# Optimization experiments

Measured on AMD Instinct MI355X. Metric: run time of the kernel, lower is better.

Reference implementation:

```python
import jax, jax.numpy as jnp
import numpy as np

EPS = 1e-5
K = 3
N_TAP = K * K


def _bn(x, g, b, m, v):
    # eval-mode batchnorm over channel axis 1 of NCHW
    inv = g / jnp.sqrt(v + EPS)
    return x * inv[None, :, None, None] + (b - m * inv)[None, :, None, None]


def _silu(x):
    return x * jax.nn.sigmoid(x)


def _dcn(x, offset, mask, w, b, pad=1):
    """Modulated deformable conv (DCNv2), stride 1.
    x: [B,C,H,W], offset: [B,2n,H,W] ((dy,dx) per tap), mask: [B,n,H,W],
    w: [O,C,K,K], b: [O]."""
    B, C, H, W = x.shape
    O = w.shape[0]
    ky, kx = jnp.meshgrid(jnp.arange(K), jnp.arange(K), indexing='ij')
    ky = ky.reshape(N_TAP).astype(x.dtype)
    kx = kx.reshape(N_TAP).astype(x.dtype)
    off = offset.reshape(B, N_TAP, 2, H, W)
    base_y = jnp.arange(H, dtype=x.dtype)[None, None, :, None]
    base_x = jnp.arange(W, dtype=x.dtype)[None, None, None, :]
    # fractional sample positions [B,n,H,W]
    py = base_y - pad + ky[None, :, None, None] + off[:, :, 0]
    px = base_x - pad + kx[None, :, None, None] + off[:, :, 1]
    y0 = jnp.floor(py)
    x0 = jnp.floor(px)
    fy = py - y0
    fx = px - x0
    y0i = y0.astype(jnp.int32)
    x0i = x0.astype(jnp.int32)
    x_flat = x.reshape(B, C, 1, H * W)

    def corner(yi, xi, wgt):
        valid = (yi >= 0) & (yi < H) & (xi >= 0) & (xi < W)
        idx = (jnp.clip(yi, 0, H - 1) * W + jnp.clip(xi, 0, W - 1)).reshape(B, 1, N_TAP, H * W)
        v = jnp.take_along_axis(x_flat, idx, axis=-1)  # [B,C,n,HW]
        return v * (wgt * valid.astype(x.dtype)).reshape(B, 1, N_TAP, H * W)

    acc = corner(y0i, x0i, (1 - fy) * (1 - fx))
    acc = acc + corner(y0i, x0i + 1, (1 - fy) * fx)
    acc = acc + corner(y0i + 1, x0i, fy * (1 - fx))
    acc = acc + corner(y0i + 1, x0i + 1, fy * fx)
    val = acc.reshape(B, C, N_TAP, H, W) * mask[:, None]  # modulation
    out = jnp.einsum('bcnhw,ocn->bohw', val, w.reshape(O, C, N_TAP))
    return out + b[None, :, None, None]


def setup_inputs() -> dict:
    key = jax.random.key(0)
    ks = jax.random.split(key, 16)
    B, C1, H, W = 8, 256, 80, 80
    C2 = 256
    Ch = 128  # c_ = int(c2 * 0.5)
    d = {}
    d['x'] = jax.random.normal(ks[0], (B, C1, H, W), jnp.float32)
    # cv1: 1x1 conv (no bias) + BN
    d['cv1_w'] = jax.random.normal(ks[1], (Ch, C1), jnp.float32) * (1.0 / np.sqrt(C1))
    d['bn1_g'] = jax.random.uniform(ks[2], (Ch,), jnp.float32, 0.5, 1.5)
    d['bn1_b'] = jax.random.normal(ks[3], (Ch,), jnp.float32) * 0.1
    d['bn1_m'] = jax.random.normal(ks[4], (Ch,), jnp.float32) * 0.1
    d['bn1_v'] = jax.random.uniform(ks[5], (Ch,), jnp.float32, 0.5, 1.5)
    # offset/mask predictor 3x3 conv (small weights -> modest deformation)
    d['off_w'] = jax.random.normal(ks[6], (3 * N_TAP, Ch, K, K), jnp.float32) * 0.01
    d['off_b'] = jnp.zeros((3 * N_TAP,), jnp.float32)
    # dcn main weight/bias
    d['dcn_w'] = jax.random.normal(ks[7], (Ch, Ch, K, K), jnp.float32) * (1.0 / np.sqrt(Ch * N_TAP))
    d['dcn_b'] = jnp.zeros((Ch,), jnp.float32)
    d['bn2_g'] = jax.random.uniform(ks[8], (Ch,), jnp.float32, 0.5, 1.5)
    d['bn2_b'] = jax.random.normal(ks[9], (Ch,), jnp.float32) * 0.1
    d['bn2_m'] = jax.random.normal(ks[10], (Ch,), jnp.float32) * 0.1
    d['bn2_v'] = jax.random.uniform(ks[11], (Ch,), jnp.float32, 0.5, 1.5)
    # cv2: 1x1 conv (no bias) + BN
    d['cv2_w'] = jax.random.normal(ks[12], (C2, Ch), jnp.float32) * (1.0 / np.sqrt(Ch))
    d['bn3_g'] = jax.random.uniform(ks[13], (C2,), jnp.float32, 0.5, 1.5)
    d['bn3_b'] = jax.random.normal(ks[14], (C2,), jnp.float32) * 0.1
    d['bn3_m'] = jax.random.normal(ks[15], (C2,), jnp.float32) * 0.1
    d['bn3_v'] = jnp.ones((C2,), jnp.float32)
    return d


def reference(x, cv1_w, bn1_g, bn1_b, bn1_m, bn1_v,
              off_w, off_b, dcn_w, dcn_b, bn2_g, bn2_b, bn2_m, bn2_v,
              cv2_w, bn3_g, bn3_b, bn3_m, bn3_v):
    # cv1: 1x1 conv -> BN -> SiLU
    y = _silu(_bn(jnp.einsum('bchw,oc->bohw', x, cv1_w), bn1_g, bn1_b, bn1_m, bn1_v))
    # offset/mask predictor: 3x3 conv, pad 1
    raw = jax.lax.conv_general_dilated(
        y, off_w, window_strides=(1, 1), padding=((1, 1), (1, 1)),
        dimension_numbers=('NCHW', 'OIHW', 'NCHW')) + off_b[None, :, None, None]
    offset = raw[:, :2 * N_TAP]
    mask = jax.nn.sigmoid(raw[:, 2 * N_TAP:])
    # modulated deformable 3x3 conv -> BN -> SiLU
    y = _silu(_bn(_dcn(y, offset, mask, dcn_w, dcn_b), bn2_g, bn2_b, bn2_m, bn2_v))
    # cv2: 1x1 conv -> BN -> SiLU
    y = _silu(_bn(jnp.einsum('bchw,oc->bohw', y, cv2_w), bn3_g, bn3_b, bn3_m, bn3_v))
    return x + y  # shortcut (c1 == c2)
```

## Files before the change

kernel.cpp:

```cpp
#include <hip/hip_runtime.h>
#include <math.h>

#define HWSZ 6400
#define WIMG 80
#define HIMG 80
#define BEPS 1e-5f

typedef __attribute__((ext_vector_type(8))) short short8;
typedef __attribute__((ext_vector_type(4))) short s16x4;
typedef __attribute__((ext_vector_type(4))) float f32x4;
typedef __attribute__((ext_vector_type(4))) int i32x4;

__device__ __forceinline__ unsigned short f2b(float f) {
    unsigned u = __builtin_bit_cast(unsigned, f);
    u += 0x7fffu + ((u >> 16) & 1u);
    return (unsigned short)(u >> 16);
}
__device__ __forceinline__ int f2b_pk(float flo, float fhi) {
    unsigned lo = __builtin_bit_cast(unsigned, flo);
    unsigned hi = __builtin_bit_cast(unsigned, fhi);
    lo += 0x7fffu + ((lo >> 16) & 1u);
    hi += 0x7fffu + ((hi >> 16) & 1u);
    return (int)__builtin_amdgcn_perm(hi, lo, 0x07060302u);
}
__device__ __forceinline__ float b2f(unsigned short h) {
    unsigned u = ((unsigned)h) << 16;
    return __builtin_bit_cast(float, u);
}
__device__ __forceinline__ float silu_f(float t) { return t / (1.f + __expf(-t)); }

#define BPOS(sub, nt, n16, q) (((((sub)*4 + (nt))*16 + (n16))*40) + (q)*8)
#define BPOS32(sub, nt, n16, oct) (((((sub)*2 + (nt))*16 + (n16))*40) + (oct)*8)

__global__ __launch_bounds__(256) void k_prep(
    const float* __restrict__ cv1w, const float* __restrict__ g1, const float* __restrict__ b1,
    const float* __restrict__ m1, const float* __restrict__ v1,
    const float* __restrict__ offw, const float* __restrict__ offb,
    const float* __restrict__ dcnw, const float* __restrict__ dcnb,
    const float* __restrict__ g2, const float* __restrict__ b2,
    const float* __restrict__ m2, const float* __restrict__ v2,
    const float* __restrict__ cv2w, const float* __restrict__ g3, const float* __restrict__ b3,
    const float* __restrict__ m3, const float* __restrict__ v3,
    unsigned short* __restrict__ apk1, unsigned short* __restrict__ apko,
    unsigned short* __restrict__ apkd, unsigned short* __restrict__ apk2,
    float* __restrict__ bias1, float* __restrict__ biaso,
    float* __restrict__ bias2, float* __restrict__ bias3)
{
    int idx = blockIdx.x * 256 + threadIdx.x;
    if (idx < 32768) {
        int j = idx & 7, L = (idx >> 3) & 63, ks = (idx >> 9) & 7, mt = idx >> 12;
        int o = mt * 16 + (L & 15), k = ks * 32 + (L >> 4) * 8 + j;
        float inv = g1[o] * rsqrtf(v1[o] + BEPS);
        apk1[idx] = f2b(cv1w[o * 256 + k] * inv);
    } else if (idx < 69632) {
        int t = idx - 32768;
        int j = t & 7, L = (t >> 3) & 63;
        int mt = t / 18432, rem = t % 18432, ks = rem >> 9;
        int o = mt * 16 + (L & 15);
        int kp = ks * 32 + (L >> 4) * 8 + j;
        int n = kp >> 7, c = kp & 127;
        float wv = (o < 27) ? offw[(size_t)(o * 128 + c) * 9 + n] : 0.f;
        apko[t] = f2b(wv);
    } else if (idx < 217088) {
        int t = idx - 69632;
        int j = t & 7, L = (t >> 3) & 63;
        int mt = t / 18432, rem = t % 18432, ks = rem >> 9;
        int o = mt * 16 + (L & 15);
        int kp = ks * 32 + (L >> 4) * 8 + j;
        int n = kp >> 7, c = kp & 127;
        float inv = g2[o] * rsqrtf(v2[o] + BEPS);
        apkd[t] = f2b(dcnw[(size_t)(o * 128 + c) * 9 + n] * inv);
    } else if (idx < 249856) {
        int t = idx - 217088;
        int j = t & 7, L = (t >> 3) & 63, ks = (t >> 9) & 3, mt = t >> 11;
        int o = mt * 16 + (L & 15), k = ks * 32 + (L >> 4) * 8 + j;
        float inv = g3[o] * rsqrtf(v3[o] + BEPS);
        apk2[t] = f2b(cv2w[o * 128 + k] * inv);
    } else if (idx < 250395) {
        int t = idx - 249856;
        if (t < 128) { float inv = g1[t] * rsqrtf(v1[t] + BEPS); bias1[t] = b1[t] - m1[t] * inv; }
        else if (t < 155) { biaso[t - 128] = offb[t - 128]; }
        else if (t < 283) { int o = t - 155; float inv = g2[o] * rsqrtf(v2[o] + BEPS);
                            bias2[o] = dcnb[o] * inv + b2[o] - m2[o] * inv; }
        else { int o = t - 283; float inv = g3[o] * rsqrtf(v3[o] + BEPS); bias3[o] = b3[o] - m3[o] * inv; }
    }
}

__global__ __launch_bounds__(256) void k_cv1(
    const float* __restrict__ x, const unsigned short* __restrict__ apk1,
    const float* __restrict__ bias1, unsigned short* __restrict__ y1t)
{
    int blk = blockIdx.x;
    int b = blk & 7, pt = blk >> 3;
    int p0 = pt * 64;
    int tid = threadIdx.x;
    int lane = tid & 63, w = tid >> 6;
    int n16 = lane & 15, qd = lane >> 4;
    int px = p0 + w * 16 + n16;
    const float* xb = x + (size_t)b * 256 * HWSZ + px;
    f32x4 acc[8];
#pragma unroll
    for (int mt = 0; mt < 8; ++mt) acc[mt] = (f32x4){0.f, 0.f, 0.f, 0.f};
#pragma unroll
    for (int ks = 0; ks < 8; ++ks) {
        float xv[8];
#pragma unroll
        for (int j = 0; j < 8; ++j)
            xv[j] = xb[(size_t)(ks * 32 + qd * 8 + j) * HWSZ];
        i32x4 bi;
#pragma unroll
        for (int t = 0; t < 4; ++t) bi[t] = f2b_pk(xv[2 * t], xv[2 * t + 1]);
        short8 bf = __builtin_bit_cast(short8, bi);
#pragma unroll
        for (int mt = 0; mt < 8; ++mt) {
            short8 af = *(const short8*)&apk1[(size_t)((mt * 8 + ks) * 64 + lane) * 8];
            acc[mt] = __builtin_amdgcn_mfma_f32_16x16x32_bf16(af, bf, acc[mt], 0, 0, 0);
        }
    }
    unsigned short* ytb = y1t + ((size_t)b * HWSZ + px) * 128;
#pragma unroll
    for (int mt = 0; mt < 8; ++mt) {
        int o0 = mt * 16 + qd * 4;
        s16x4 v;
#pragma unroll
        for (int r = 0; r < 4; ++r)
            v[r] = (short)f2b(silu_f(acc[mt][r] + bias1[o0 + r]));
        *(s16x4*)&ytb[o0] = v;
    }
}

__global__ __launch_bounds__(256) void k_off(
    const unsigned short* __restrict__ y1t, const unsigned short* __restrict__ apko,
    const float* __restrict__ biaso, float* __restrict__ raw)
{
    int blk = blockIdx.x;
    int b = blk & 7, pt = blk >> 3;
    int p0 = pt * 64;
    int tid = threadIdx.x;
    int lane = tid & 63, w = tid >> 6;
    int n16 = lane & 15, qd = lane >> 4;
    int pxl = w * 16 + n16;
    int p = p0 + pxl;
    int h = p / WIMG, wx = p % WIMG;
    const unsigned short* yb = y1t + (size_t)b * HWSZ * 128 + qd * 8;
    f32x4 acc[2];
    acc[0] = (f32x4){0.f, 0.f, 0.f, 0.f};
    acc[1] = (f32x4){0.f, 0.f, 0.f, 0.f};
    const short8 zz = {0, 0, 0, 0, 0, 0, 0, 0};
#pragma unroll
    for (int n = 0; n < 9; ++n) {
        int hh = h - 1 + n / 3, ww = wx - 1 + n % 3;
        bool valid = ((unsigned)hh < HIMG) && ((unsigned)ww < WIMG);
        int spx = valid ? hh * WIMG + ww : 0;
        const unsigned short* ys = yb + (size_t)spx * 128;
        short8 v[4];
#pragma unroll
        for (int sub = 0; sub < 4; ++sub) {
            v[sub] = *(const short8*)&ys[sub * 32];
            if (!valid) v[sub] = zz;
        }
#pragma unroll
        for (int sub = 0; sub < 4; ++sub) {
            int ks = n * 4 + sub;
            short8 af0 = *(const short8*)&apko[(size_t)(ks * 64 + lane) * 8];
            short8 af1 = *(const short8*)&apko[(size_t)((36 + ks) * 64 + lane) * 8];
            acc[0] = __builtin_amdgcn_mfma_f32_16x16x32_bf16(af0, v[sub], acc[0], 0, 0, 0);
            acc[1] = __builtin_amdgcn_mfma_f32_16x16x32_bf16(af1, v[sub], acc[1], 0, 0, 0);
        }
    }
    float* rb = raw + (size_t)b * 27 * HWSZ + p0 + w * 16 + n16;
#pragma unroll
    for (int mi = 0; mi < 2; ++mi)
#pragma unroll
        for (int r = 0; r < 4; ++r) {
            int o = mi * 16 + qd * 4 + r;
            if (o < 27) {
                float t = acc[mi][r] + biaso[o];
                if (o >= 18) t = 1.f / (1.f + __expf(-t));
                rb[(size_t)o * HWSZ] = t;
            }
        }
}

__global__ __launch_bounds__(256) void k_dcn(
    const unsigned short* __restrict__ y1t, const float* __restrict__ raw,
    const unsigned short* __restrict__ apkd, const float* __restrict__ bias2,
    unsigned short* __restrict__ zt)
{
    __shared__ float swgt[4][9][32];
    __shared__ unsigned short sidx[4][9][32];
    __shared__ __align__(16) unsigned short sV[5120];
    int blk = blockIdx.x;
    int b = blk & 7, pt = blk >> 3;
    int p0 = pt * 32;
    int tid = threadIdx.x;

    for (int i = tid; i < 288; i += 256) {
        int n = i >> 5, pp = i & 31;
        int p = p0 + pp;
        int h = p / WIMG, wx = p % WIMG;
        const float* rb = raw + (size_t)b * 27 * HWSZ + p;
        float dy = rb[(size_t)(2 * n) * HWSZ];
        float dx = rb[(size_t)(2 * n + 1) * HWSZ];
        float mk = rb[(size_t)(18 + n) * HWSZ];
        float py = (float)(h - 1 + n / 3) + dy;
        float px = (float)(wx - 1 + n % 3) + dx;
        float y0f = floorf(py), x0f = floorf(px);
        float fy = py - y0f, fx = px - x0f;
        int y0 = (int)y0f, x0 = (int)x0f;
#pragma unroll
        for (int k = 0; k < 4; ++k) {
            int yy = y0 + (k >> 1);
            int xx = x0 + (k & 1);
            bool valid = ((unsigned)yy < HIMG) && ((unsigned)xx < WIMG);
            float wk = ((k >> 1) ? fy : 1.f - fy) * ((k & 1) ? fx : 1.f - fx);
            wk = valid ? wk * mk : 0.f;
            int yc = min(max(yy, 0), HIMG - 1);
            int xc = min(max(xx, 0), WIMG - 1);
            sidx[k][n][pp] = (unsigned short)(yc * WIMG + xc);
            swgt[k][n][pp] = wk;
        }
    }
    __syncthreads();

    int lane = tid & 63, w = tid >> 6;
    int n16 = lane & 15, qd = lane >> 4;
    int pxl = tid >> 3, q8 = tid & 7;
    int gsub = q8 >> 1;
    int goct = (q8 & 1) * 2;
    const unsigned short* yb = y1t + (size_t)b * HWSZ * 128;
    f32x4 acc[2][2];
#pragma unroll
    for (int mi = 0; mi < 2; ++mi)
#pragma unroll
        for (int nt = 0; nt < 2; ++nt) acc[mi][nt] = (f32x4){0.f, 0.f, 0.f, 0.f};

    for (int n = 0; n < 9; ++n) {
        float av[2][8];
#pragma unroll
        for (int s = 0; s < 2; ++s)
#pragma unroll
            for (int j = 0; j < 8; ++j) av[s][j] = 0.f;
#pragma unroll
        for (int k = 0; k < 4; ++k) {
            float wk = swgt[k][n][pxl];
            const unsigned short* ys = yb + (size_t)sidx[k][n][pxl] * 128 + q8 * 16;
            short8 v0 = *(const short8*)&ys[0];
            short8 v1 = *(const short8*)&ys[8];
#pragma unroll
            for (int j = 0; j < 8; ++j) {
                av[0][j] = fmaf(wk, b2f((unsigned short)v0[j]), av[0][j]);
                av[1][j] = fmaf(wk, b2f((unsigned short)v1[j]), av[1][j]);
            }
        }
#pragma unroll
        for (int s = 0; s < 2; ++s) {
            short8 v;
#pragma unroll
            for (int j = 0; j < 8; ++j) v[j] = (short)f2b(av[s][j]);
            *(short8*)&sV[BPOS32(gsub, pxl >> 4, pxl & 15, goct + s)] = v;
        }
        __syncthreads();
#pragma unroll
        for (int sub = 0; sub < 4; ++sub) {
            int ks = n * 4 + sub;
            short8 bf[2];
#pragma unroll
            for (int nt = 0; nt < 2; ++nt)
                bf[nt] = *(const short8*)&sV[BPOS32(sub, nt, n16, qd)];
#pragma unroll
            for (int mi = 0; mi < 2; ++mi) {
                short8 af = *(const short8*)&apkd[(size_t)(((2 * w + mi) * 36 + ks) * 64 + lane) * 8];
#pragma unroll
                for (int nt = 0; nt < 2; ++nt)
                    acc[mi][nt] = __builtin_amdgcn_mfma_f32_16x16x32_bf16(af, bf[nt], acc[mi][nt], 0, 0, 0);
            }
        }
        __syncthreads();
    }
    unsigned short* zb = zt + ((size_t)b * HWSZ + p0) * 128;
#pragma unroll
    for (int mi = 0; mi < 2; ++mi)
#pragma unroll
        for (int nt = 0; nt < 2; ++nt) {
            int o0 = (2 * w + mi) * 16 + qd * 4;
            int px = nt * 16 + n16;
            s16x4 v;
#pragma unroll
            for (int r = 0; r < 4; ++r)
                v[r] = (short)f2b(silu_f(acc[mi][nt][r] + bias2[o0 + r]));
            *(s16x4*)&zb[(size_t)px * 128 + o0] = v;
        }
}

__global__ __launch_bounds__(256) void k_cv2(
    const unsigned short* __restrict__ zt, const float* __restrict__ x,
    const unsigned short* __restrict__ apk2, const float* __restrict__ bias3,
    float* __restrict__ out)
{
    int blk = blockIdx.x;
    int b = blk & 7, pt = blk >> 3;
    int p0 = pt * 32;
    int tid = threadIdx.x;
    int lane = tid & 63, w = tid >> 6;
    int n16 = lane & 15, qd = lane >> 4;
    const unsigned short* zb = zt + ((size_t)b * HWSZ + p0) * 128;
    f32x4 acc[2][4];
#pragma unroll
    for (int mt = 0; mt < 2; ++mt)
#pragma unroll
        for (int ntl = 0; ntl < 4; ++ntl) acc[mt][ntl] = (f32x4){0.f, 0.f, 0.f, 0.f};
#pragma unroll
    for (int ks = 0; ks < 4; ++ks) {
        short8 az[2];
#pragma unroll
        for (int mt = 0; mt < 2; ++mt)
            az[mt] = *(const short8*)&zb[(size_t)(mt * 16 + n16) * 128 + ks * 32 + qd * 8];
#pragma unroll
        for (int ntl = 0; ntl < 4; ++ntl) {
            int nt = w * 4 + ntl;
            short8 bw = *(const short8*)&apk2[(size_t)((nt * 4 + ks) * 64 + lane) * 8];
#pragma unroll
            for (int mt = 0; mt < 2; ++mt)
                acc[mt][ntl] = __builtin_amdgcn_mfma_f32_16x16x32_bf16(az[mt], bw, acc[mt][ntl], 0, 0, 0);
        }
    }
    const float* xb = x + (size_t)b * 256 * HWSZ;
    float* ob = out + (size_t)b * 256 * HWSZ;
#pragma unroll
    for (int mt = 0; mt < 2; ++mt) {
        int px = p0 + mt * 16 + qd * 4;
#pragma unroll
        for (int ntl = 0; ntl < 4; ++ntl) {
            int o = (w * 4 + ntl) * 16 + n16;
            float bv = bias3[o];
            size_t base = (size_t)o * HWSZ + px;
            float4 xv = *(const float4*)&xb[base];
            float4 r;
            r.x = xv.x + silu_f(acc[mt][ntl][0] + bv);
            r.y = xv.y + silu_f(acc[mt][ntl][1] + bv);
            r.z = xv.z + silu_f(acc[mt][ntl][2] + bv);
            r.w = xv.w + silu_f(acc[mt][ntl][3] + bv);
            *(float4*)&ob[base] = r;
        }
    }
}

extern "C" void kernel_launch(void* const* d_in, const int* in_sizes, int n_in,
                              void* d_out, int out_size, void* d_ws, size_t ws_size,
                              hipStream_t stream) {
    const float* x     = (const float*)d_in[0];
    const float* cv1w  = (const float*)d_in[1];
    const float* bn1g  = (const float*)d_in[2];
    const float* bn1b  = (const float*)d_in[3];
    const float* bn1m  = (const float*)d_in[4];
    const float* bn1v  = (const float*)d_in[5];
    const float* offw  = (const float*)d_in[6];
    const float* offb  = (const float*)d_in[7];
    const float* dcnw  = (const float*)d_in[8];
    const float* dcnb  = (const float*)d_in[9];
    const float* bn2g  = (const float*)d_in[10];
    const float* bn2b  = (const float*)d_in[11];
    const float* bn2m  = (const float*)d_in[12];
    const float* bn2v  = (const float*)d_in[13];
    const float* cv2w  = (const float*)d_in[14];
    const float* bn3g  = (const float*)d_in[15];
    const float* bn3b  = (const float*)d_in[16];
    const float* bn3m  = (const float*)d_in[17];
    const float* bn3v  = (const float*)d_in[18];
    float* out = (float*)d_out;

    float* base = (float*)d_ws;
    unsigned short* y1t = (unsigned short*)base;
    float* raw   = base + 3276800;
    unsigned short* zt  = (unsigned short*)(base + 4659200);
    unsigned short* apk1 = (unsigned short*)(base + 7936000);
    unsigned short* apko = (unsigned short*)(base + 7952384);
    unsigned short* apkd = (unsigned short*)(base + 7970816);
    unsigned short* apk2 = (unsigned short*)(base + 8044544);
    float* bias1 = base + 8060928;
    float* biaso = base + 8061056;
    float* bias2 = base + 8061088;
    float* bias3 = base + 8061216;

    k_prep<<<979, 256, 0, stream>>>(cv1w, bn1g, bn1b, bn1m, bn1v,
                                    offw, offb, dcnw, dcnb,
                                    bn2g, bn2b, bn2m, bn2v,
                                    cv2w, bn3g, bn3b, bn3m, bn3v,
                                    apk1, apko, apkd, apk2,
                                    bias1, biaso, bias2, bias3);
    k_cv1<<<800, 256, 0, stream>>>(x, apk1, bias1, y1t);
    k_off<<<800, 256, 0, stream>>>(y1t, apko, biaso, raw);
    k_dcn<<<1600, 256, 0, stream>>>(y1t, raw, apkd, bias2, zt);
    k_cv2<<<1600, 256, 0, stream>>>(zt, x, apk2, bias3, out);
}
```

Baseline: 239.1 us.

## Fuse offset conv into DCN kernel and triple-buffer gathered taps

Moves the offset/mask 3x3 conv into the DCN kernel: two waves compute the 27 raw channels for the block's 32 pixels into shared memory. This removes the separate kernel launch and the global round-trip of the raw buffer. The tap loop is also restructured with a 3-slot shared buffer so the gather for the next tap overlaps the MFMAs of the current one, and one barrier per tap is dropped. The LDS layout gets a per-sub pad to avoid bank conflicts. The cost is that two of the four waves do the offset conv while the other two sit idle, and LDS use per block grows.

```diff
diff --git a/kernel.cpp b/kernel.cpp
--- a/kernel.cpp
+++ b/kernel.cpp
@@ -29,8 +29,8 @@
 }
 __device__ __forceinline__ float silu_f(float t) { return t / (1.f + __expf(-t)); }
 
-#define BPOS(sub, nt, n16, q) (((((sub)*4 + (nt))*16 + (n16))*40) + (q)*8)
-#define BPOS32(sub, nt, n16, oct) (((((sub)*2 + (nt))*16 + (n16))*40) + (oct)*8)
+#define BPOS32(sub, nt, n16, oct) (((((sub)*2 + (nt))*16 + (n16))*40) + (oct)*8 + (sub)*8)
+#define SVBUF 5184
 
 __global__ __launch_bounds__(256) void k_prep(
     const float* __restrict__ cv1w, const float* __restrict__ g1, const float* __restrict__ b1,
@@ -129,80 +129,75 @@
     }
 }
 
-__global__ __launch_bounds__(256) void k_off(
-    const unsigned short* __restrict__ y1t, const unsigned short* __restrict__ apko,
-    const float* __restrict__ biaso, float* __restrict__ raw)
-{
-    int blk = blockIdx.x;
-    int b = blk & 7, pt = blk >> 3;
-    int p0 = pt * 64;
-    int tid = threadIdx.x;
-    int lane = tid & 63, w = tid >> 6;
-    int n16 = lane & 15, qd = lane >> 4;
-    int pxl = w * 16 + n16;
-    int p = p0 + pxl;
-    int h = p / WIMG, wx = p % WIMG;
-    const unsigned short* yb = y1t + (size_t)b * HWSZ * 128 + qd * 8;
-    f32x4 acc[2];
-    acc[0] = (f32x4){0.f, 0.f, 0.f, 0.f};
-    acc[1] = (f32x4){0.f, 0.f, 0.f, 0.f};
-    const short8 zz = {0, 0, 0, 0, 0, 0, 0, 0};
-#pragma unroll
-    for (int n = 0; n < 9; ++n) {
-        int hh = h - 1 + n / 3, ww = wx - 1 + n % 3;
-        bool valid = ((unsigned)hh < HIMG) && ((unsigned)ww < WIMG);
-        int spx = valid ? hh * WIMG + ww : 0;
-        const unsigned short* ys = yb + (size_t)spx * 128;
-        short8 v[4];
-#pragma unroll
-        for (int sub = 0; sub < 4; ++sub) {
-            v[sub] = *(const short8*)&ys[sub * 32];
-            if (!valid) v[sub] = zz;
-        }
-#pragma unroll
-        for (int sub = 0; sub < 4; ++sub) {
-            int ks = n * 4 + sub;
-            short8 af0 = *(const short8*)&apko[(size_t)(ks * 64 + lane) * 8];
-            short8 af1 = *(const short8*)&apko[(size_t)((36 + ks) * 64 + lane) * 8];
-            acc[0] = __builtin_amdgcn_mfma_f32_16x16x32_bf16(af0, v[sub], acc[0], 0, 0, 0);
-            acc[1] = __builtin_amdgcn_mfma_f32_16x16x32_bf16(af1, v[sub], acc[1], 0, 0, 0);
-        }
-    }
-    float* rb = raw + (size_t)b * 27 * HWSZ + p0 + w * 16 + n16;
-#pragma unroll
-    for (int mi = 0; mi < 2; ++mi)
-#pragma unroll
-        for (int r = 0; r < 4; ++r) {
-            int o = mi * 16 + qd * 4 + r;
-            if (o < 27) {
-                float t = acc[mi][r] + biaso[o];
-                if (o >= 18) t = 1.f / (1.f + __expf(-t));
-                rb[(size_t)o * HWSZ] = t;
-            }
-        }
-}
-
 __global__ __launch_bounds__(256) void k_dcn(
-    const unsigned short* __restrict__ y1t, const float* __restrict__ raw,
+    const unsigned short* __restrict__ y1t,
+    const unsigned short* __restrict__ apko, const float* __restrict__ biaso,
     const unsigned short* __restrict__ apkd, const float* __restrict__ bias2,
     unsigned short* __restrict__ zt)
 {
+    __shared__ float rawL[27 * 33];
     __shared__ float swgt[4][9][32];
     __shared__ unsigned short sidx[4][9][32];
-    __shared__ __align__(16) unsigned short sV[5120];
+    __shared__ __align__(16) unsigned short sV[3 * SVBUF];
     int blk = blockIdx.x;
     int b = blk & 7, pt = blk >> 3;
     int p0 = pt * 32;
     int tid = threadIdx.x;
+    int lane = tid & 63, w = tid >> 6;
+    int n16 = lane & 15, qd = lane >> 4;
+    const unsigned short* yb = y1t + (size_t)b * HWSZ * 128;
+
+    if (w < 2) {
+        int pxa = w * 16 + n16;
+        int p = p0 + pxa;
+        int h = p / WIMG, wx = p % WIMG;
+        const unsigned short* ybq = yb + qd * 8;
+        f32x4 oacc[2];
+        oacc[0] = (f32x4){0.f, 0.f, 0.f, 0.f};
+        oacc[1] = (f32x4){0.f, 0.f, 0.f, 0.f};
+        const short8 zz = {0, 0, 0, 0, 0, 0, 0, 0};
+#pragma unroll
+        for (int n = 0; n < 9; ++n) {
+            int hh = h - 1 + n / 3, ww = wx - 1 + n % 3;
+            bool valid = ((unsigned)hh < HIMG) && ((unsigned)ww < WIMG);
+            int spx = valid ? hh * WIMG + ww : 0;
+            const unsigned short* ys = ybq + (size_t)spx * 128;
+            short8 v[4];
+#pragma unroll
+            for (int sub = 0; sub < 4; ++sub) {
+                v[sub] = *(const short8*)&ys[sub * 32];
+                if (!valid) v[sub] = zz;
+            }
+#pragma unroll
+            for (int sub = 0; sub < 4; ++sub) {
+                int ks = n * 4 + sub;
+                short8 af0 = *(const short8*)&apko[(size_t)(ks * 64 + lane) * 8];
+                short8 af1 = *(const short8*)&apko[(size_t)((36 + ks) * 64 + lane) * 8];
+                oacc[0] = __builtin_amdgcn_mfma_f32_16x16x32_bf16(af0, v[sub], oacc[0], 0, 0, 0);
+                oacc[1] = __builtin_amdgcn_mfma_f32_16x16x32_bf16(af1, v[sub], oacc[1], 0, 0, 0);
+            }
+        }
+#pragma unroll
+        for (int mi = 0; mi < 2; ++mi)
+#pragma unroll
+            for (int r = 0; r < 4; ++r) {
+                int o = mi * 16 + qd * 4 + r;
+                if (o < 27) {
+                    float t = oacc[mi][r] + biaso[o];
+                    if (o >= 18) t = 1.f / (1.f + __expf(-t));
+                    rawL[o * 33 + pxa] = t;
+                }
+            }
+    }
+    __syncthreads();
 
     for (int i = tid; i < 288; i += 256) {
         int n = i >> 5, pp = i & 31;
         int p = p0 + pp;
         int h = p / WIMG, wx = p % WIMG;
-        const float* rb = raw + (size_t)b * 27 * HWSZ + p;
-        float dy = rb[(size_t)(2 * n) * HWSZ];
-        float dx = rb[(size_t)(2 * n + 1) * HWSZ];
-        float mk = rb[(size_t)(18 + n) * HWSZ];
+        float dy = rawL[(2 * n) * 33 + pp];
+        float dx = rawL[(2 * n + 1) * 33 + pp];
+        float mk = rawL[(18 + n) * 33 + pp];
         float py = (float)(h - 1 + n / 3) + dy;
         float px = (float)(wx - 1 + n % 3) + dx;
         float y0f = floorf(py), x0f = floorf(px);
@@ -223,24 +218,19 @@
     }
     __syncthreads();
 
-    int lane = tid & 63, w = tid >> 6;
-    int n16 = lane & 15, qd = lane >> 4;
     int pxl = tid >> 3, q8 = tid & 7;
     int gsub = q8 >> 1;
     int goct = (q8 & 1) * 2;
-    const unsigned short* yb = y1t + (size_t)b * HWSZ * 128;
     f32x4 acc[2][2];
 #pragma unroll
     for (int mi = 0; mi < 2; ++mi)
 #pragma unroll
         for (int nt = 0; nt < 2; ++nt) acc[mi][nt] = (f32x4){0.f, 0.f, 0.f, 0.f};
 
-    for (int n = 0; n < 9; ++n) {
-        float av[2][8];
-#pragma unroll
-        for (int s = 0; s < 2; ++s)
-#pragma unroll
-            for (int j = 0; j < 8; ++j) av[s][j] = 0.f;
+    auto gather_tap = [&](int n, int bsel) {
+        float av0[8], av1[8];
+#pragma unroll
+        for (int j = 0; j < 8; ++j) { av0[j] = 0.f; av1[j] = 0.f; }
 #pragma unroll
         for (int k = 0; k < 4; ++k) {
             float wk = swgt[k][n][pxl];
@@ -249,25 +239,30 @@
             short8 v1 = *(const short8*)&ys[8];
 #pragma unroll
             for (int j = 0; j < 8; ++j) {
-                av[0][j] = fmaf(wk, b2f((unsigned short)v0[j]), av[0][j]);
-                av[1][j] = fmaf(wk, b2f((unsigned short)v1[j]), av[1][j]);
-            }
-        }
-#pragma unroll
-        for (int s = 0; s < 2; ++s) {
-            short8 v;
-#pragma unroll
-            for (int j = 0; j < 8; ++j) v[j] = (short)f2b(av[s][j]);
-            *(short8*)&sV[BPOS32(gsub, pxl >> 4, pxl & 15, goct + s)] = v;
-        }
+                av0[j] = fmaf(wk, b2f((unsigned short)v0[j]), av0[j]);
+                av1[j] = fmaf(wk, b2f((unsigned short)v1[j]), av1[j]);
+            }
+        }
+        short8 o0, o1;
+#pragma unroll
+        for (int j = 0; j < 8; ++j) { o0[j] = (short)f2b(av0[j]); o1[j] = (short)f2b(av1[j]); }
+        unsigned short* dst = &sV[bsel * SVBUF + BPOS32(gsub, pxl >> 4, pxl & 15, goct)];
+        *(short8*)dst = o0;
+        *(short8*)(dst + 8) = o1;
+    };
+
+    gather_tap(0, 0);
+    for (int n = 0; n < 9; ++n) {
+        if (n < 8) gather_tap(n + 1, (n + 1) % 3);
         __syncthreads();
+        int bb = (n % 3) * SVBUF;
 #pragma unroll
         for (int sub = 0; sub < 4; ++sub) {
             int ks = n * 4 + sub;
             short8 bf[2];
 #pragma unroll
             for (int nt = 0; nt < 2; ++nt)
-                bf[nt] = *(const short8*)&sV[BPOS32(sub, nt, n16, qd)];
+                bf[nt] = *(const short8*)&sV[bb + BPOS32(sub, nt, n16, qd)];
 #pragma unroll
             for (int mi = 0; mi < 2; ++mi) {
                 short8 af = *(const short8*)&apkd[(size_t)(((2 * w + mi) * 36 + ks) * 64 + lane) * 8];
@@ -276,8 +271,8 @@
                     acc[mi][nt] = __builtin_amdgcn_mfma_f32_16x16x32_bf16(af, bf[nt], acc[mi][nt], 0, 0, 0);
             }
         }
-        __syncthreads();
-    }
+    }
+
     unsigned short* zb = zt + ((size_t)b * HWSZ + p0) * 128;
 #pragma unroll
     for (int mi = 0; mi < 2; ++mi)
@@ -372,16 +367,15 @@
 
     float* base = (float*)d_ws;
     unsigned short* y1t = (unsigned short*)base;
-    float* raw   = base + 3276800;
-    unsigned short* zt  = (unsigned short*)(base + 4659200);
-    unsigned short* apk1 = (unsigned short*)(base + 7936000);
-    unsigned short* apko = (unsigned short*)(base + 7952384);
-    unsigned short* apkd = (unsigned short*)(base + 7970816);
-    unsigned short* apk2 = (unsigned short*)(base + 8044544);
-    float* bias1 = base + 8060928;
-    float* biaso = base + 8061056;
-    float* bias2 = base + 8061088;
-    float* bias3 = base + 8061216;
+    unsigned short* zt  = (unsigned short*)(base + 3276800);
+    unsigned short* apk1 = (unsigned short*)(base + 6553600);
+    unsigned short* apko = (unsigned short*)(base + 6569984);
+    unsigned short* apkd = (unsigned short*)(base + 6588416);
+    unsigned short* apk2 = (unsigned short*)(base + 6662144);
+    float* bias1 = base + 6678528;
+    float* biaso = base + 6678656;
+    float* bias2 = base + 6678688;
+    float* bias3 = base + 6678816;
 
     k_prep<<<979, 256, 0, stream>>>(cv1w, bn1g, bn1b, bn1m, bn1v,
                                     offw, offb, dcnw, dcnb,
@@ -390,7 +384,6 @@
                                     apk1, apko, apkd, apk2,
                                     bias1, biaso, bias2, bias3);
     k_cv1<<<800, 256, 0, stream>>>(x, apk1, bias1, y1t);
-    k_off<<<800, 256, 0, stream>>>(y1t, apko, biaso, raw);
-    k_dcn<<<1600, 256, 0, stream>>>(y1t, raw, apkd, bias2, zt);
+    k_dcn<<<1600, 256, 0, stream>>>(y1t, apko, biaso, apkd, bias2, zt);
     k_cv2<<<1600, 256, 0, stream>>>(zt, x, apk2, bias3, out);
 }
```

Result: no change. 239.2 us (+0.0%).
